# Performance work log

Measured on AMD Instinct MI355X. Metric: run time of the kernel, lower is better.

## Reference

```python
import jax, jax.numpy as jnp
import numpy as np

N = 100000
E = 1600000
F_IN = 128
HDIM = 64
HEADS = 8
C1 = HDIM // HEADS  # 8 per-head channels in conv1
NUM_CLASSES = 2
NUM_GRAPHS = 64
NEG_SLOPE = 0.2


def setup_inputs() -> dict:
    key = jax.random.key(0)
    ks = jax.random.split(key, 12)
    x = jax.random.normal(ks[0], (N, F_IN), dtype=jnp.float32)
    edge_index = jax.random.randint(ks[1], (2, E), 0, N, dtype=jnp.int64)
    batch = jnp.sort(jax.random.randint(ks[2], (N,), 0, NUM_GRAPHS, dtype=jnp.int64))
    # conv1 params (Glorot-ish scale)
    W1 = jax.random.normal(ks[3], (F_IN, HEADS * C1), dtype=jnp.float32) * (1.0 / np.sqrt(F_IN))
    att_src1 = jax.random.normal(ks[4], (HEADS, C1), dtype=jnp.float32) * 0.1
    att_dst1 = jax.random.normal(ks[5], (HEADS, C1), dtype=jnp.float32) * 0.1
    b1 = jnp.zeros((HEADS * C1,), dtype=jnp.float32)
    # conv2 params (1 head, no concat)
    W2 = jax.random.normal(ks[6], (HDIM, 1 * NUM_CLASSES), dtype=jnp.float32) * (1.0 / np.sqrt(HDIM))
    att_src2 = jax.random.normal(ks[7], (1, NUM_CLASSES), dtype=jnp.float32) * 0.1
    att_dst2 = jax.random.normal(ks[8], (1, NUM_CLASSES), dtype=jnp.float32) * 0.1
    b2 = jnp.zeros((NUM_CLASSES,), dtype=jnp.float32)
    return {"x": x, "edge_index": edge_index, "batch": batch,
            "W1": W1, "att_src1": att_src1, "att_dst1": att_dst1, "b1": b1,
            "W2": W2, "att_src2": att_src2, "att_dst2": att_dst2, "b2": b2}


def gat_conv(x, src, dst, W, a_src, a_dst, b, heads, ch, concat):
    # PyG GATConv: linear proj -> per-edge attention -> segment softmax over dst -> scatter-add
    n = x.shape[0]
    h = (x @ W).reshape(n, heads, ch)                      # [N,H,C]
    alpha_s = jnp.einsum('nhc,hc->nh', h, a_src)           # [N,H]
    alpha_d = jnp.einsum('nhc,hc->nh', h, a_dst)           # [N,H]
    e = jax.nn.leaky_relu(alpha_s[src] + alpha_d[dst], NEG_SLOPE)  # [E,H]
    m = jax.ops.segment_max(e, dst, num_segments=n)        # stable softmax per dst
    e = jnp.exp(e - m[dst])
    denom = jax.ops.segment_sum(e, dst, num_segments=n) + 1e-16
    alpha = e / denom[dst]                                 # [E,H]
    msg = h[src] * alpha[:, :, None]                       # [E,H,C]
    out = jax.ops.segment_sum(msg, dst, num_segments=n)    # [N,H,C]
    if concat:
        out = out.reshape(n, heads * ch)
    else:
        out = out.mean(axis=1)
    return out + b


def reference(x, edge_index, batch, W1, att_src1, att_dst1, b1, W2, att_src2, att_dst2, b2):
    # PyG GATConv default add_self_loops=True
    loops = jnp.arange(N, dtype=edge_index.dtype)
    src = jnp.concatenate([edge_index[0], loops])
    dst = jnp.concatenate([edge_index[1], loops])
    h = gat_conv(x, src, dst, W1, att_src1, att_dst1, b1, HEADS, C1, concat=True)
    h = jax.nn.relu(h)
    # F.dropout with training=False (eval mode) -> identity
    h = gat_conv(h, src, dst, W2, att_src2, att_dst2, b2, 1, NUM_CLASSES, concat=False)
    # global_mean_pool over batch ids
    sums = jax.ops.segment_sum(h, batch, num_segments=NUM_GRAPHS)
    cnts = jax.ops.segment_sum(jnp.ones((N,), h.dtype), batch, num_segments=NUM_GRAPHS)
    pooled = sums / jnp.maximum(cnts, 1.0)[:, None]        # [G, num_classes]
    return jax.nn.log_softmax(pooled, axis=1)
```

## Files before the change

kernel.cpp:

```cpp
#include <hip/hip_runtime.h>
#include <hip/hip_bf16.h>
#include <hip/hip_fp16.h>
#include <math.h>

#define NN 100000
#define EE 1600000
#define ET 1700000
#define NEG_SLOPE 0.2f
#define XS_STRIDE 136

#define BKB 8
#define BKSZ 256
#define NBUCK 391
#define SLAB 8192
#define PAD 32
#define EPT2 16
#define CHUNK2 (256 * EPT2)
#define NCH2 ((ET + CHUNK2 - 1) / CHUNK2)

typedef _Float16 f16;
typedef f16 f16x8 __attribute__((ext_vector_type(8)));
typedef float f32x4 __attribute__((ext_vector_type(4)));
typedef float f32x2 __attribute__((ext_vector_type(2)));

__device__ __forceinline__ float leaky(float v) {
    return v > 0.f ? v : NEG_SLOPE * v;
}
__device__ __forceinline__ unsigned char enc_fp8(float v) {
    int pk = __builtin_amdgcn_cvt_pk_fp8_f32(v, 0.f, 0, false);
    return (unsigned char)(pk & 0xff);
}

__global__ __launch_bounds__(256) void convert_w_kernel(
        const float* __restrict__ W1, f16* __restrict__ wt) {
    int i = blockIdx.x * 256 + threadIdx.x;
    if (i < 128 * 64) {
        int n = i >> 7, k = i & 127;
        wt[n * 128 + k] = (f16)W1[k * 64 + n];
    }
}

__global__ __launch_bounds__(256) void gemm1_mfma(
        const float* __restrict__ x, const f16* __restrict__ wt,
        const float* __restrict__ att_s, const float* __restrict__ att_d,
        unsigned char* __restrict__ h1f8, __half* __restrict__ as1h,
        float* __restrict__ ad1o) {
    __shared__ f16 xs[64 * XS_STRIDE];
    const int tid = threadIdx.x;
    const int node0 = blockIdx.x * 64;
    for (int i = tid; i < 64 * 64; i += 256) {
        int r = i >> 6, cp = i & 63;
        int n = node0 + r;
        float2 v = (n < NN) ? ((const float2*)x)[(long)n * 64 + cp]
                            : make_float2(0.f, 0.f);
        xs[r * XS_STRIDE + 2 * cp]     = (f16)v.x;
        xs[r * XS_STRIDE + 2 * cp + 1] = (f16)v.y;
    }
    __syncthreads();
    const int wv = tid >> 6;
    const int lane = tid & 63;
    const int n16 = lane & 15;
    const int quad = lane >> 4;
    f16x8 bf[4][4];
#pragma unroll
    for (int t = 0; t < 4; ++t)
#pragma unroll
        for (int kk = 0; kk < 4; ++kk)
            bf[t][kk] = *(const f16x8*)(wt + ((t * 16 + n16) * 128 + kk * 32 + quad * 8));
    f32x4 acc[4] = {{0,0,0,0},{0,0,0,0},{0,0,0,0},{0,0,0,0}};
#pragma unroll
    for (int kk = 0; kk < 4; ++kk) {
        f16x8 af = *(const f16x8*)(xs + ((wv * 16 + n16) * XS_STRIDE + kk * 32 + quad * 8));
#pragma unroll
        for (int t = 0; t < 4; ++t)
            acc[t] = __builtin_amdgcn_mfma_f32_16x16x32_f16(af, bf[t][kk], acc[t], 0, 0, 0);
    }
    float ats[4], atd[4];
#pragma unroll
    for (int t = 0; t < 4; ++t) {
        ats[t] = att_s[t * 16 + n16];
        atd[t] = att_d[t * 16 + n16];
    }
#pragma unroll
    for (int t = 0; t < 4; ++t)
#pragma unroll
        for (int r = 0; r < 4; ++r) {
            int m = node0 + wv * 16 + quad * 4 + r;
            bool ok = (m < NN);
            if (ok) h1f8[m * 64 + t * 16 + n16] = enc_fp8(acc[t][r]);
            float vs = acc[t][r] * ats[t];
            float vd = acc[t][r] * atd[t];
            vs += __shfl_xor(vs, 1, 64); vd += __shfl_xor(vd, 1, 64);
            vs += __shfl_xor(vs, 2, 64); vd += __shfl_xor(vd, 2, 64);
            vs += __shfl_xor(vs, 4, 64); vd += __shfl_xor(vd, 4, 64);
            if (ok && (n16 & 7) == 0) {
                int h = t * 2 + (n16 >> 3);
                as1h[m * 8 + h] = __float2half_rn(vs);
                ad1o[m * 8 + h] = vd;
            }
        }
}

__global__ __launch_bounds__(256) void bucket_fill(
        const int* __restrict__ ei, int* __restrict__ bcur,
        unsigned* __restrict__ gpay) {
    __shared__ int lcnt[NBUCK];
    __shared__ int gbase[NBUCK];
    const int tid = threadIdx.x;
    for (int i = tid; i < NBUCK; i += 256) lcnt[i] = 0;
    __syncthreads();
    const int base = blockIdx.x * CHUNK2 + tid;
    unsigned pay[EPT2];
    int bk[EPT2], pos[EPT2];
#pragma unroll
    for (int k = 0; k < EPT2; ++k) {
        int e = base + k * 256;
        if (e < ET) {
            int s, d;
            if (e < EE) {
                s = __builtin_nontemporal_load(ei + e);
                d = __builtin_nontemporal_load(ei + EE + e);
            } else { s = d = e - EE; }
            int b = d >> BKB;
            bk[k] = b;
            pay[k] = ((unsigned)(d & (BKSZ - 1)) << 17) | (unsigned)s;
            pos[k] = atomicAdd(&lcnt[b], 1);
        } else bk[k] = -1;
    }
    __syncthreads();
    for (int i = tid; i < NBUCK; i += 256)
        gbase[i] = lcnt[i] ? (i * SLAB + atomicAdd(&bcur[i * PAD], lcnt[i])) : 0;
    __syncthreads();
#pragma unroll
    for (int k = 0; k < EPT2; ++k)
        if (bk[k] >= 0) gpay[gbase[bk[k]] + pos[k]] = pay[k];
}

__global__ __launch_bounds__(256) void fine_csr(
        const unsigned* __restrict__ gpay, const int* __restrict__ bcur,
        int* __restrict__ rowptr, int* __restrict__ rowend,
        int* __restrict__ csr_src) {
    __shared__ int cnt[BKSZ];
    __shared__ int ts[256];
    const int b = blockIdx.x;
    const int tid = threadIdx.x;
    const int off = b * SLAB;
    int blen = bcur[b * PAD];
    if (blen > SLAB) blen = SLAB;
    const int d0 = b << BKB;
    cnt[tid] = 0;
    __syncthreads();
    for (int i = tid; i < blen; i += 256)
        atomicAdd(&cnt[gpay[off + i] >> 17], 1);
    __syncthreads();
    int v = cnt[tid];
    ts[tid] = v;
    __syncthreads();
    for (int o = 1; o < 256; o <<= 1) {
        int u = (tid >= o) ? ts[tid - o] : 0;
        __syncthreads();
        ts[tid] += u;
        __syncthreads();
    }
    int excl = ts[tid] - v;
    cnt[tid] = excl;
    int d = d0 + tid;
    if (d < NN) {
        rowptr[d] = off + excl;
        rowend[d] = off + excl + v;
    }
    __syncthreads();
    for (int i = tid; i < blen; i += 256) {
        unsigned pay = gpay[off + i];
        int pos = atomicAdd(&cnt[pay >> 17], 1);
        csr_src[off + pos] = (int)(pay & 0x1FFFFu);
    }
}

__global__ __launch_bounds__(256) void conv1_fused_kernel(
        const int* __restrict__ rowptr, const int* __restrict__ rowend,
        const int* __restrict__ csr_src, const __half* __restrict__ as1h,
        const float* __restrict__ ad1,
        const unsigned char* __restrict__ h1f8, const float* __restrict__ b1,
        const float* __restrict__ W2, const float* __restrict__ as2,
        const float* __restrict__ ad2, float4* __restrict__ rec) {
    const int tid = threadIdx.x;
    const int wv = tid >> 6;
    const int c = tid & 63;
    const int slot = c >> 3;
    const int hd = c & 7;
    int n0 = __builtin_amdgcn_readfirstlane((blockIdx.x * 4 + wv) * 2);
    int n1 = n0 + 1;
    const float adA = ad1[n0 * 8 + hd];
    const float adB = ad1[n1 * 8 + hd];
    int jA = rowptr[n0], eA = rowend[n0];
    int jB = rowptr[n1], eB = rowend[n1];
    float accA[8] = {0.f,0.f,0.f,0.f,0.f,0.f,0.f,0.f};
    float accB[8] = {0.f,0.f,0.f,0.f,0.f,0.f,0.f,0.f};
    float lA = 0.f, lB = 0.f;

#define STEP1(j, e, ad, l, acc)                                              \
    {                                                                        \
        int rem = (e) - (j);                                                 \
        int sl = slot < rem ? slot : rem - 1;                                \
        int src = csr_src[(j) + sl];                                         \
        float p = __expf(leaky(__half2float(as1h[src * 8 + hd]) + (ad)));    \
        if (slot >= rem) p = 0.f;                                            \
        uint2 fb = *(const uint2*)(h1f8 + src * 64 + hd * 8);                \
        f32x2 f01 = __builtin_amdgcn_cvt_pk_f32_fp8((int)fb.x, 0);           \
        f32x2 f23 = __builtin_amdgcn_cvt_pk_f32_fp8((int)fb.x, 1);           \
        f32x2 f45 = __builtin_amdgcn_cvt_pk_f32_fp8((int)fb.y, 0);           \
        f32x2 f67 = __builtin_amdgcn_cvt_pk_f32_fp8((int)fb.y, 1);           \
        (l) += p;                                                            \
        acc[0] += p * f01.x; acc[1] += p * f01.y;                            \
        acc[2] += p * f23.x; acc[3] += p * f23.y;                            \
        acc[4] += p * f45.x; acc[5] += p * f45.y;                            \
        acc[6] += p * f67.x; acc[7] += p * f67.y;                            \
        (j) += 8;                                                            \
    }

    while (jA < eA && jB < eB) {
        STEP1(jA, eA, adA, lA, accA);
        STEP1(jB, eB, adB, lB, accB);
    }
    while (jA < eA) STEP1(jA, eA, adA, lA, accA);
    while (jB < eB) STEP1(jB, eB, adB, lB, accB);
#undef STEP1

#pragma unroll
    for (int off = 8; off <= 32; off <<= 1) {
        lA += __shfl_xor(lA, off, 64);
        lB += __shfl_xor(lB, off, 64);
#pragma unroll
        for (int i = 0; i < 8; ++i) {
            accA[i] += __shfl_xor(accA[i], off, 64);
            accB[i] += __shfl_xor(accB[i], off, 64);
        }
    }
    const float invA = 1.f / (lA + 1e-16f);
    const float invB = 1.f / (lB + 1e-16f);
    const float4* b1v = (const float4*)(b1 + hd * 8);
    const float4* w2v = (const float4*)(W2 + hd * 16);
    float bb[8], ww[16];
    *(float4*)(bb)     = b1v[0]; *(float4*)(bb + 4)  = b1v[1];
    *(float4*)(ww)     = w2v[0]; *(float4*)(ww + 4)  = w2v[1];
    *(float4*)(ww + 8) = w2v[2]; *(float4*)(ww + 12) = w2v[3];
    float rA0 = 0.f, rA1 = 0.f, rB0 = 0.f, rB1 = 0.f;
#pragma unroll
    for (int i = 0; i < 8; ++i) {
        float aAv = accA[i] * invA + bb[i];
        float aBv = accB[i] * invB + bb[i];
        aAv = aAv > 0.f ? aAv : 0.f;
        aBv = aBv > 0.f ? aBv : 0.f;
        rA0 += aAv * ww[2 * i];
        rA1 += aAv * ww[2 * i + 1];
        rB0 += aBv * ww[2 * i];
        rB1 += aBv * ww[2 * i + 1];
    }
#pragma unroll
    for (int off = 1; off <= 4; off <<= 1) {
        rA0 += __shfl_xor(rA0, off, 64);
        rA1 += __shfl_xor(rA1, off, 64);
        rB0 += __shfl_xor(rB0, off, 64);
        rB1 += __shfl_xor(rB1, off, 64);
    }
    if (c == 0) {
        rec[n0] = make_float4(rA0 * as2[0] + rA1 * as2[1], rA0, rA1,
                              rA0 * ad2[0] + rA1 * ad2[1]);
        rec[n1] = make_float4(rB0 * as2[0] + rB1 * as2[1], rB0, rB1,
                              rB0 * ad2[0] + rB1 * ad2[1]);
    }
}

__global__ __launch_bounds__(256) void conv2_pool_kernel(
        const int* __restrict__ rowptr, const int* __restrict__ rowend,
        const int* __restrict__ csr_src, const float4* __restrict__ rec,
        const int* __restrict__ batch,
        float* __restrict__ pooled ) {
    __shared__ float ls[192];
    int tid = threadIdx.x;
    if (tid < 192) ls[tid] = 0.f;
    __syncthreads();
    int n = blockIdx.x * 256 + tid;
    if (n < NN) {
        float adn = rec[n].w;
        int jb = rowptr[n], je = rowend[n];
        float l0 = 0.f, l1 = 0.f, l2 = 0.f, l3 = 0.f;
        float x0 = 0.f, x1 = 0.f, x2 = 0.f, x3 = 0.f;
        float y0 = 0.f, y1 = 0.f, y2 = 0.f, y3 = 0.f;
        int j = jb;
        for (; j + 3 < je; j += 4) {
            float4 ra = rec[csr_src[j]];
            float4 rb = rec[csr_src[j + 1]];
            float4 rc = rec[csr_src[j + 2]];
            float4 rd = rec[csr_src[j + 3]];
            float pa = __expf(leaky(ra.x + adn));
            float pb = __expf(leaky(rb.x + adn));
            float pc = __expf(leaky(rc.x + adn));
            float pd = __expf(leaky(rd.x + adn));
            l0 += pa; x0 += pa * ra.y; y0 += pa * ra.z;
            l1 += pb; x1 += pb * rb.y; y1 += pb * rb.z;
            l2 += pc; x2 += pc * rc.y; y2 += pc * rc.z;
            l3 += pd; x3 += pd * rd.y; y3 += pd * rd.z;
        }
        for (; j < je; ++j) {
            float4 ra = rec[csr_src[j]];
            float pa = __expf(leaky(ra.x + adn));
            l0 += pa; x0 += pa * ra.y; y0 += pa * ra.z;
        }
        float l = (l0 + l1) + (l2 + l3);
        float xx = (x0 + x1) + (x2 + x3);
        float yy = (y0 + y1) + (y2 + y3);
        float inv = 1.f / (l + 1e-16f);
        int g = batch[n];
        atomicAdd(&ls[g * 2],     xx * inv);
        atomicAdd(&ls[g * 2 + 1], yy * inv);
        atomicAdd(&ls[128 + g],   1.f);
    }
    __syncthreads();
    if (tid < 192) atomicAdd(&pooled[tid], ls[tid]);
}

__global__ __launch_bounds__(64) void final_kernel(
        const float* __restrict__ pooled, const float* __restrict__ b2,
        float* __restrict__ out) {
    int g = threadIdx.x;
    if (g >= 64) return;
    float c = pooled[128 + g];
    float denom = c > 1.f ? c : 1.f;
    float p0 = pooled[g * 2] / denom + b2[0];
    float p1 = pooled[g * 2 + 1] / denom + b2[1];
    float m = fmaxf(p0, p1);
    float lse = m + logf(expf(p0 - m) + expf(p1 - m));
    out[g * 2] = p0 - lse;
    out[g * 2 + 1] = p1 - lse;
}

extern "C" void kernel_launch(void* const* d_in, const int* in_sizes, int n_in,
                              void* d_out, int out_size, void* d_ws, size_t ws_size,
                              hipStream_t stream) {
    const float* x   = (const float*)d_in[0];
    const int*   ei  = (const int*)d_in[1];
    const int*   bat = (const int*)d_in[2];
    const float* W1  = (const float*)d_in[3];
    const float* as1 = (const float*)d_in[4];
    const float* ad1 = (const float*)d_in[5];
    const float* b1  = (const float*)d_in[6];
    const float* W2  = (const float*)d_in[7];
    const float* as2 = (const float*)d_in[8];
    const float* ad2 = (const float*)d_in[9];
    const float* b2  = (const float*)d_in[10];
    float* out = (float*)d_out;

    float* ws = (float*)d_ws;
    const long off_h1f8   = 0;
    const long off_wt     = off_h1f8 + (long)NN * 16;
    const long off_as1h   = off_wt   + 4096;
    const long off_ad1    = off_as1h + (long)NN * 4;
    const long off_rec    = off_ad1  + (long)NN * 8;
    const long off_rowptr = off_rec  + (long)NN * 4;
    const long off_rowend = off_rowptr + NN;
    const long off_gpay   = off_rowend + NN;
    const long off_csr    = off_gpay + (long)NBUCK * SLAB;
    const long off_zero   = off_csr  + (long)NBUCK * SLAB;
    const long off_bcur   = off_zero;
    const long off_pool   = off_bcur + NBUCK * PAD;
    const long zero_elems = off_pool + 192 - off_zero;

    hipMemsetAsync(ws + off_zero, 0, zero_elems * sizeof(float), stream);

    convert_w_kernel<<<32, 256, 0, stream>>>(W1, (f16*)(ws + off_wt));
    gemm1_mfma<<<(NN + 63) / 64, 256, 0, stream>>>(
        x, (const f16*)(ws + off_wt), as1, ad1,
        (unsigned char*)(ws + off_h1f8), (__half*)(ws + off_as1h),
        ws + off_ad1);

    bucket_fill<<<NCH2, 256, 0, stream>>>(ei, (int*)(ws + off_bcur),
                                          (unsigned*)(ws + off_gpay));
    fine_csr<<<NBUCK, 256, 0, stream>>>(
        (const unsigned*)(ws + off_gpay), (const int*)(ws + off_bcur),
        (int*)(ws + off_rowptr), (int*)(ws + off_rowend),
        (int*)(ws + off_csr));

    conv1_fused_kernel<<<NN / 8, 256, 0, stream>>>(
        (const int*)(ws + off_rowptr), (const int*)(ws + off_rowend),
        (const int*)(ws + off_csr), (const __half*)(ws + off_as1h),
        ws + off_ad1, (const unsigned char*)(ws + off_h1f8),
        b1, W2, as2, ad2, (float4*)(ws + off_rec));

    conv2_pool_kernel<<<(NN + 255) / 256, 256, 0, stream>>>(
        (const int*)(ws + off_rowptr), (const int*)(ws + off_rowend),
        (const int*)(ws + off_csr), (const float4*)(ws + off_rec),
        bat, ws + off_pool);

    final_kernel<<<1, 64, 0, stream>>>(ws + off_pool, b2, out);
}
```

Measured before the change: 236.7 us.

## Pack per-node fp8 features and attention logits into one 128-byte record

Interleaves each node's fp8 head features, half-precision source logit and float destination logit into a single 16-byte per-head record, so each edge gather in conv1 is one uint4 load instead of separate feature and logit loads. CSR rows are padded to multiples of 8 using a dummy node whose logit is -inf, which removes the per-slot bounds clamping and masking in the inner loop. Logits are prescaled by log2(e) so exp2f can replace __expf, and the post-aggregation reduction is rewritten as a halving butterfly so each lane ends up owning one channel. Padding adds wasted gathers on short rows, and it falls back to unpadded rows when the slab would overflow.

```diff
diff --git a/kernel.cpp b/kernel.cpp
--- a/kernel.cpp
+++ b/kernel.cpp
@@ -8,6 +8,7 @@
 #define ET 1700000
 #define NEG_SLOPE 0.2f
 #define XS_STRIDE 136
+#define L2E 1.44269504088896f
 
 #define BKB 8
 #define BKSZ 256
@@ -31,20 +32,25 @@
     return (unsigned char)(pk & 0xff);
 }
 
+
 __global__ __launch_bounds__(256) void convert_w_kernel(
-        const float* __restrict__ W1, f16* __restrict__ wt) {
+        const float* __restrict__ W1, f16* __restrict__ wt,
+        unsigned char* __restrict__ nrec) {
     int i = blockIdx.x * 256 + threadIdx.x;
     if (i < 128 * 64) {
         int n = i >> 7, k = i & 127;
         wt[n * 128 + k] = (f16)W1[k * 64 + n];
     }
+    if (blockIdx.x == 0 && threadIdx.x < 8) {
+        uint4* dr = (uint4*)(nrec + (size_t)NN * 128);
+        dr[threadIdx.x] = make_uint4(0u, 0u, 0xFC00u, 0u);
+    }
 }
 
 __global__ __launch_bounds__(256) void gemm1_mfma(
         const float* __restrict__ x, const f16* __restrict__ wt,
         const float* __restrict__ att_s, const float* __restrict__ att_d,
-        unsigned char* __restrict__ h1f8, __half* __restrict__ as1h,
-        float* __restrict__ ad1o) {
+        unsigned char* __restrict__ nrec) {
     __shared__ f16 xs[64 * XS_STRIDE];
     const int tid = threadIdx.x;
     const int node0 = blockIdx.x * 64;
@@ -81,22 +87,26 @@
         ats[t] = att_s[t * 16 + n16];
         atd[t] = att_d[t * 16 + n16];
     }
+    const int head = (n16 >> 3);
+    const int chpos = n16 & 7;
 #pragma unroll
     for (int t = 0; t < 4; ++t)
 #pragma unroll
         for (int r = 0; r < 4; ++r) {
             int m = node0 + wv * 16 + quad * 4 + r;
             bool ok = (m < NN);
-            if (ok) h1f8[m * 64 + t * 16 + n16] = enc_fp8(acc[t][r]);
+            if (ok)
+                nrec[(size_t)m * 128 + (t * 2 + head) * 16 + chpos] =
+                    enc_fp8(acc[t][r]);
             float vs = acc[t][r] * ats[t];
             float vd = acc[t][r] * atd[t];
             vs += __shfl_xor(vs, 1, 64); vd += __shfl_xor(vd, 1, 64);
             vs += __shfl_xor(vs, 2, 64); vd += __shfl_xor(vd, 2, 64);
             vs += __shfl_xor(vs, 4, 64); vd += __shfl_xor(vd, 4, 64);
-            if (ok && (n16 & 7) == 0) {
-                int h = t * 2 + (n16 >> 3);
-                as1h[m * 8 + h] = __float2half_rn(vs);
-                ad1o[m * 8 + h] = vd;
+            if (ok && chpos == 0) {
+                unsigned char* nb = nrec + (size_t)m * 128 + (t * 2 + head) * 16;
+                *(__half*)(nb + 8)  = __float2half_rn(vs * L2E);
+                *(float*)(nb + 12) = vd * L2E;
             }
         }
 }
@@ -154,7 +164,8 @@
         atomicAdd(&cnt[gpay[off + i] >> 17], 1);
     __syncthreads();
     int v = cnt[tid];
-    ts[tid] = v;
+    int vp = (v + 7) & ~7;
+    ts[tid] = vp;
     __syncthreads();
     for (int o = 1; o < 256; o <<= 1) {
         int u = (tid >= o) ? ts[tid - o] : 0;
@@ -162,13 +173,15 @@
         ts[tid] += u;
         __syncthreads();
     }
-    int excl = ts[tid] - v;
+    int excl = ts[tid] - vp;
+    if (excl + vp > SLAB) vp = v;
     cnt[tid] = excl;
     int d = d0 + tid;
     if (d < NN) {
         rowptr[d] = off + excl;
         rowend[d] = off + excl + v;
     }
+    for (int i = v; i < vp; ++i) csr_src[off + excl + i] = NN;
     __syncthreads();
     for (int i = tid; i < blen; i += 256) {
         unsigned pay = gpay[off + i];
@@ -179,11 +192,10 @@
 
 __global__ __launch_bounds__(256) void conv1_fused_kernel(
         const int* __restrict__ rowptr, const int* __restrict__ rowend,
-        const int* __restrict__ csr_src, const __half* __restrict__ as1h,
-        const float* __restrict__ ad1,
-        const unsigned char* __restrict__ h1f8, const float* __restrict__ b1,
-        const float* __restrict__ W2, const float* __restrict__ as2,
-        const float* __restrict__ ad2, float4* __restrict__ rec) {
+        const int* __restrict__ csr_src, const unsigned char* __restrict__ nrec,
+        const float* __restrict__ b1, const float* __restrict__ W2,
+        const float* __restrict__ as2, const float* __restrict__ ad2,
+        float4* __restrict__ rec) {
     const int tid = threadIdx.x;
     const int wv = tid >> 6;
     const int c = tid & 63;
@@ -191,26 +203,27 @@
     const int hd = c & 7;
     int n0 = __builtin_amdgcn_readfirstlane((blockIdx.x * 4 + wv) * 2);
     int n1 = n0 + 1;
-    const float adA = ad1[n0 * 8 + hd];
-    const float adB = ad1[n1 * 8 + hd];
-    int jA = rowptr[n0], eA = rowend[n0];
-    int jB = rowptr[n1], eB = rowend[n1];
+    const float adA = *(const float*)(nrec + ((size_t)n0 << 7) + (hd << 4) + 12);
+    const float adB = *(const float*)(nrec + ((size_t)n1 << 7) + (hd << 4) + 12);
+    int jA = rowptr[n0];
+    int jB = rowptr[n1];
+    int eA = jA + ((rowend[n0] - jA + 7) & ~7);
+    int eB = jB + ((rowend[n1] - jB + 7) & ~7);
     float accA[8] = {0.f,0.f,0.f,0.f,0.f,0.f,0.f,0.f};
     float accB[8] = {0.f,0.f,0.f,0.f,0.f,0.f,0.f,0.f};
     float lA = 0.f, lB = 0.f;
 
-#define STEP1(j, e, ad, l, acc)                                              \
+#define STEP1(j, ad, l, acc)                                                 \
     {                                                                        \
-        int rem = (e) - (j);                                                 \
-        int sl = slot < rem ? slot : rem - 1;                                \
-        int src = csr_src[(j) + sl];                                         \
-        float p = __expf(leaky(__half2float(as1h[src * 8 + hd]) + (ad)));    \
-        if (slot >= rem) p = 0.f;                                            \
-        uint2 fb = *(const uint2*)(h1f8 + src * 64 + hd * 8);                \
-        f32x2 f01 = __builtin_amdgcn_cvt_pk_f32_fp8((int)fb.x, 0);           \
-        f32x2 f23 = __builtin_amdgcn_cvt_pk_f32_fp8((int)fb.x, 1);           \
-        f32x2 f45 = __builtin_amdgcn_cvt_pk_f32_fp8((int)fb.y, 0);           \
-        f32x2 f67 = __builtin_amdgcn_cvt_pk_f32_fp8((int)fb.y, 1);           \
+        int src = csr_src[(j) + slot];                                       \
+        uint4 v = *(const uint4*)(nrec + (((size_t)src << 7) | (hd << 4)));  \
+        unsigned short ush = (unsigned short)v.z;                            \
+        float as = __half2float(*(const __half*)&ush);                       \
+        float p = exp2f(leaky(as + (ad)));                                   \
+        f32x2 f01 = __builtin_amdgcn_cvt_pk_f32_fp8((int)v.x, 0);            \
+        f32x2 f23 = __builtin_amdgcn_cvt_pk_f32_fp8((int)v.x, 1);            \
+        f32x2 f45 = __builtin_amdgcn_cvt_pk_f32_fp8((int)v.y, 0);            \
+        f32x2 f67 = __builtin_amdgcn_cvt_pk_f32_fp8((int)v.y, 1);            \
         (l) += p;                                                            \
         acc[0] += p * f01.x; acc[1] += p * f01.y;                            \
         acc[2] += p * f23.x; acc[3] += p * f23.y;                            \
@@ -220,55 +233,63 @@
     }
 
     while (jA < eA && jB < eB) {
-        STEP1(jA, eA, adA, lA, accA);
-        STEP1(jB, eB, adB, lB, accB);
-    }
-    while (jA < eA) STEP1(jA, eA, adA, lA, accA);
-    while (jB < eB) STEP1(jB, eB, adB, lB, accB);
+        STEP1(jA, adA, lA, accA);
+        STEP1(jB, adB, lB, accB);
+    }
+    while (jA < eA) STEP1(jA, adA, lA, accA);
+    while (jB < eB) STEP1(jB, adB, lB, accB);
 #undef STEP1
 
-#pragma unroll
-    for (int off = 8; off <= 32; off <<= 1) {
-        lA += __shfl_xor(lA, off, 64);
-        lB += __shfl_xor(lB, off, 64);
-#pragma unroll
-        for (int i = 0; i < 8; ++i) {
-            accA[i] += __shfl_xor(accA[i], off, 64);
-            accB[i] += __shfl_xor(accB[i], off, 64);
-        }
-    }
-    const float invA = 1.f / (lA + 1e-16f);
-    const float invB = 1.f / (lB + 1e-16f);
-    const float4* b1v = (const float4*)(b1 + hd * 8);
-    const float4* w2v = (const float4*)(W2 + hd * 16);
-    float bb[8], ww[16];
-    *(float4*)(bb)     = b1v[0]; *(float4*)(bb + 4)  = b1v[1];
-    *(float4*)(ww)     = w2v[0]; *(float4*)(ww + 4)  = w2v[1];
-    *(float4*)(ww + 8) = w2v[2]; *(float4*)(ww + 12) = w2v[3];
-    float rA0 = 0.f, rA1 = 0.f, rB0 = 0.f, rB1 = 0.f;
-#pragma unroll
-    for (int i = 0; i < 8; ++i) {
-        float aAv = accA[i] * invA + bb[i];
-        float aBv = accB[i] * invB + bb[i];
-        aAv = aAv > 0.f ? aAv : 0.f;
-        aBv = aBv > 0.f ? aBv : 0.f;
-        rA0 += aAv * ww[2 * i];
-        rA1 += aAv * ww[2 * i + 1];
-        rB0 += aBv * ww[2 * i];
-        rB1 += aBv * ww[2 * i + 1];
-    }
-#pragma unroll
-    for (int off = 1; off <= 4; off <<= 1) {
+    const int sb0 = slot & 1, sb1 = slot & 2, sb2 = slot & 4;
+    float h4A[4], h4B[4];
+#pragma unroll
+    for (int i = 0; i < 4; ++i) {
+        float xa0 = accA[i]     + __shfl_xor(accA[i], 8, 64);
+        float xa1 = accA[i + 4] + __shfl_xor(accA[i + 4], 8, 64);
+        h4A[i] = sb0 ? xa1 : xa0;
+        float xb0 = accB[i]     + __shfl_xor(accB[i], 8, 64);
+        float xb1 = accB[i + 4] + __shfl_xor(accB[i + 4], 8, 64);
+        h4B[i] = sb0 ? xb1 : xb0;
+    }
+    float h2A[2], h2B[2];
+#pragma unroll
+    for (int i = 0; i < 2; ++i) {
+        float xa0 = h4A[i]     + __shfl_xor(h4A[i], 16, 64);
+        float xa1 = h4A[i + 2] + __shfl_xor(h4A[i + 2], 16, 64);
+        h2A[i] = sb1 ? xa1 : xa0;
+        float xb0 = h4B[i]     + __shfl_xor(h4B[i], 16, 64);
+        float xb1 = h4B[i + 2] + __shfl_xor(h4B[i + 2], 16, 64);
+        h2B[i] = sb1 ? xb1 : xb0;
+    }
+    float ya0 = h2A[0] + __shfl_xor(h2A[0], 32, 64);
+    float ya1 = h2A[1] + __shfl_xor(h2A[1], 32, 64);
+    float aA = sb2 ? ya1 : ya0;
+    float yb0 = h2B[0] + __shfl_xor(h2B[0], 32, 64);
+    float yb1 = h2B[1] + __shfl_xor(h2B[1], 32, 64);
+    float aB = sb2 ? yb1 : yb0;
+    lA += __shfl_xor(lA, 8, 64); lA += __shfl_xor(lA, 16, 64); lA += __shfl_xor(lA, 32, 64);
+    lB += __shfl_xor(lB, 8, 64); lB += __shfl_xor(lB, 16, 64); lB += __shfl_xor(lB, 32, 64);
+    int ch = (hd << 3) + ((slot & 1) << 2) + (slot & 2) + ((slot >> 2) & 1);
+    float invA = 1.f / (lA + 1e-16f);
+    float invB = 1.f / (lB + 1e-16f);
+    float bb = b1[ch];
+    float2 w = ((const float2*)W2)[ch];
+    float vA = fmaxf(aA * invA + bb, 0.f);
+    float vB = fmaxf(aB * invB + bb, 0.f);
+    float rA0 = vA * w.x, rA1 = vA * w.y;
+    float rB0 = vB * w.x, rB1 = vB * w.y;
+#pragma unroll
+    for (int off = 1; off < 64; off <<= 1) {
         rA0 += __shfl_xor(rA0, off, 64);
         rA1 += __shfl_xor(rA1, off, 64);
         rB0 += __shfl_xor(rB0, off, 64);
         rB1 += __shfl_xor(rB1, off, 64);
     }
     if (c == 0) {
-        rec[n0] = make_float4(rA0 * as2[0] + rA1 * as2[1], rA0, rA1,
-                              rA0 * ad2[0] + rA1 * ad2[1]);
-        rec[n1] = make_float4(rB0 * as2[0] + rB1 * as2[1], rB0, rB1,
-                              rB0 * ad2[0] + rB1 * ad2[1]);
+        rec[n0] = make_float4((rA0 * as2[0] + rA1 * as2[1]) * L2E, rA0, rA1,
+                              (rA0 * ad2[0] + rA1 * ad2[1]) * L2E);
+        rec[n1] = make_float4((rB0 * as2[0] + rB1 * as2[1]) * L2E, rB0, rB1,
+                              (rB0 * ad2[0] + rB1 * ad2[1]) * L2E);
     }
 }
 
@@ -294,10 +315,10 @@
             float4 rb = rec[csr_src[j + 1]];
             float4 rc = rec[csr_src[j + 2]];
             float4 rd = rec[csr_src[j + 3]];
-            float pa = __expf(leaky(ra.x + adn));
-            float pb = __expf(leaky(rb.x + adn));
-            float pc = __expf(leaky(rc.x + adn));
-            float pd = __expf(leaky(rd.x + adn));
+            float pa = exp2f(leaky(ra.x + adn));
+            float pb = exp2f(leaky(rb.x + adn));
+            float pc = exp2f(leaky(rc.x + adn));
+            float pd = exp2f(leaky(rd.x + adn));
             l0 += pa; x0 += pa * ra.y; y0 += pa * ra.z;
             l1 += pb; x1 += pb * rb.y; y1 += pb * rb.z;
             l2 += pc; x2 += pc * rc.y; y2 += pc * rc.z;
@@ -305,7 +326,7 @@
         }
         for (; j < je; ++j) {
             float4 ra = rec[csr_src[j]];
-            float pa = __expf(leaky(ra.x + adn));
+            float pa = exp2f(leaky(ra.x + adn));
             l0 += pa; x0 += pa * ra.y; y0 += pa * ra.z;
         }
         float l = (l0 + l1) + (l2 + l3);
@@ -353,27 +374,25 @@
     float* out = (float*)d_out;
 
     float* ws = (float*)d_ws;
-    const long off_h1f8   = 0;
-    const long off_wt     = off_h1f8 + (long)NN * 16;
-    const long off_as1h   = off_wt   + 4096;
-    const long off_ad1    = off_as1h + (long)NN * 4;
-    const long off_rec    = off_ad1  + (long)NN * 8;
-    const long off_rowptr = off_rec  + (long)NN * 4;
+    const long off_nrec   = 0;
+    const long off_wt     = off_nrec + (long)(NN + 1) * 32;
+    const long off_rec    = off_wt + 4096;
+    const long off_rowptr = off_rec + (long)NN * 4;
     const long off_rowend = off_rowptr + NN;
     const long off_gpay   = off_rowend + NN;
     const long off_csr    = off_gpay + (long)NBUCK * SLAB;
-    const long off_zero   = off_csr  + (long)NBUCK * SLAB;
+    const long off_zero   = off_csr + (long)NBUCK * SLAB;
     const long off_bcur   = off_zero;
     const long off_pool   = off_bcur + NBUCK * PAD;
     const long zero_elems = off_pool + 192 - off_zero;
 
     hipMemsetAsync(ws + off_zero, 0, zero_elems * sizeof(float), stream);
 
-    convert_w_kernel<<<32, 256, 0, stream>>>(W1, (f16*)(ws + off_wt));
+    convert_w_kernel<<<32, 256, 0, stream>>>(W1, (f16*)(ws + off_wt),
+                                             (unsigned char*)(ws + off_nrec));
     gemm1_mfma<<<(NN + 63) / 64, 256, 0, stream>>>(
         x, (const f16*)(ws + off_wt), as1, ad1,
-        (unsigned char*)(ws + off_h1f8), (__half*)(ws + off_as1h),
-        ws + off_ad1);
+        (unsigned char*)(ws + off_nrec));
 
     bucket_fill<<<NCH2, 256, 0, stream>>>(ei, (int*)(ws + off_bcur),
                                           (unsigned*)(ws + off_gpay));
@@ -384,8 +403,7 @@
 
     conv1_fused_kernel<<<NN / 8, 256, 0, stream>>>(
         (const int*)(ws + off_rowptr), (const int*)(ws + off_rowend),
-        (const int*)(ws + off_csr), (const __half*)(ws + off_as1h),
-        ws + off_ad1, (const unsigned char*)(ws + off_h1f8),
+        (const int*)(ws + off_csr), (const unsigned char*)(ws + off_nrec),
         b1, W2, as2, ad2, (float4*)(ws + off_rec));
 
     conv2_pool_kernel<<<(NN + 255) / 256, 256, 0, stream>>>(
```

Result: no change. 233.9 us (-1.2%).
